# Optimization experiments

Measured on AMD Instinct MI355X. Metric: run time of the kernel, lower is better.

Reference implementation:

```python
import jax, jax.numpy as jnp
import numpy as np

DIM = 128
H = 8
EXP = 4
INNER = EXP * DIM          # 512
HD = INNER // H            # 64
B, N = 4, 1024
PE_C = 32


def setup_inputs() -> dict:
    key = jax.random.key(0)
    ks = jax.random.split(key, 9)
    s = 0.02
    return {
        "x": jax.random.normal(ks[0], (B, N, DIM), jnp.float32),
        "pe": jax.random.normal(ks[1], (N, N, PE_C), jnp.float32),
        "Wq": jax.random.normal(ks[2], (INNER, DIM), jnp.float32) * s,
        "Wk": jax.random.normal(ks[3], (INNER, DIM), jnp.float32) * s,
        "Wv": jax.random.normal(ks[4], (INNER, DIM), jnp.float32) * s,
        "bv": jax.random.normal(ks[5], (INNER,), jnp.float32) * s,
        "Wproj": jax.random.normal(ks[6], (DIM, INNER), jnp.float32) * s,
        "Wpe": jax.random.normal(ks[7], (HD, PE_C), jnp.float32) * s,
        "bpe": jax.random.normal(ks[8], (HD,), jnp.float32) * s,
    }


def reference(x, pe, Wq, Wk, Wv, bv, Wproj, Wpe, bpe):
    Bsz, Nn, C = x.shape
    scale = HD ** (-0.5)
    # [B, N, inner] -> [B, H, N, hd]
    def split_heads(t):
        return t.reshape(Bsz, Nn, H, HD).transpose(0, 2, 1, 3)
    q = split_heads(x @ Wq.T)
    k = split_heads(x @ Wk.T)
    v = split_heads(x @ Wv.T + bv)
    score = jnp.einsum('bhic,bhjc->bhij', q * scale, k)   # [B,H,N,N]
    attn = jax.nn.softmax(score, axis=-1)
    out = jnp.einsum('bhij,bhjc->bhic', attn, v)           # [B,H,N,hd]
    pe_sum = jnp.einsum('bhij,ijc->bhic', attn, pe)        # [B,H,N,32]
    out = out + pe_sum @ Wpe.T + bpe                       # pe_proj
    out = out.transpose(0, 2, 1, 3).reshape(Bsz, Nn, H * HD)
    return out @ Wproj.T                                   # [B,N,dim]
```

## Files before the change

kernel.cpp:

```cpp
#include <hip/hip_runtime.h>
#include <hip/hip_bf16.h>

#define DIM   128
#define NH    8
#define INNER 512
#define HD    64
#define BSZ   4
#define NSEQ  1024
#define PEC   32
#define BH    32

typedef __attribute__((ext_vector_type(4))) float f32x4;
typedef __attribute__((ext_vector_type(2))) float f32x2;
typedef __attribute__((ext_vector_type(8))) short s16x8;
typedef __attribute__((ext_vector_type(4))) unsigned short u16x4;
typedef __attribute__((ext_vector_type(2))) unsigned int u32x2;
typedef __attribute__((ext_vector_type(4))) unsigned int u32x4;

__device__ __forceinline__ unsigned short f2bf(float f) {
    unsigned u = __float_as_uint(f);
    u += 0x7fffu + ((u >> 16) & 1u);
    return (unsigned short)(u >> 16);
}

__device__ __forceinline__ float bf2f(short s) {
    return __uint_as_float(((unsigned)(unsigned short)s) << 16);
}

__device__ __forceinline__ s16x8 load8bf(const float* p) {
    f32x4 a = *(const f32x4*)p;
    f32x4 b = *(const f32x4*)(p + 4);
    s16x8 r;
    r[0] = (short)f2bf(a[0]); r[1] = (short)f2bf(a[1]);
    r[2] = (short)f2bf(a[2]); r[3] = (short)f2bf(a[3]);
    r[4] = (short)f2bf(b[0]); r[5] = (short)f2bf(b[1]);
    r[6] = (short)f2bf(b[2]); r[7] = (short)f2bf(b[3]);
    return r;
}

__device__ __forceinline__ f32x4 mfma16(s16x8 a, s16x8 b, f32x4 c) {
    return __builtin_amdgcn_mfma_f32_16x16x32_bf16(a, b, c, 0, 0, 0);
}

__global__ __launch_bounds__(256) void k_qkv(
    const float* __restrict__ x,
    const float* __restrict__ Wq, const float* __restrict__ Wk,
    const float* __restrict__ Wv, const float* __restrict__ bv,
    unsigned short* __restrict__ qws, unsigned short* __restrict__ kws,
    unsigned short* __restrict__ vtws)
{
    __shared__ unsigned short xs[64][136];
    int lane = threadIdx.x & 63, wave = threadIdx.x >> 6;
    int lr = lane & 15, lg = lane >> 4;
    int ct   = blockIdx.x * 4 + wave;
    int col0 = ct * 16;
    int m0   = blockIdx.y * 64;

    int tid = threadIdx.x;
    #pragma unroll
    for (int it = 0; it < 4; ++it) {
        int flat = it * 256 + tid;
        int r = flat >> 4, c8 = (flat & 15) * 8;
        *(s16x8*)&xs[r][c8] = load8bf(x + (m0 + r) * DIM + c8);
    }
    __syncthreads();

    const float* W; int cbase; int which = col0 >> 9;
    if (which == 0)      { W = Wq; cbase = col0; }
    else if (which == 1) { W = Wk; cbase = col0 - 512; }
    else                 { W = Wv; cbase = col0 - 1024; }

    const float* wrow = W + (cbase + lr) * DIM;
    s16x8 bfr[4];
    #pragma unroll
    for (int kt = 0; kt < 4; ++kt) bfr[kt] = load8bf(wrow + kt * 32 + lg * 8);

    if (which == 2) {
        int colW = cbase + lr;
        int h = colW >> 6, d = colW & 63;
        float bias = bv[colW];
        #pragma unroll
        for (int ms = 0; ms < 4; ++ms) {
            f32x4 acc = {0.f, 0.f, 0.f, 0.f};
            #pragma unroll
            for (int kt = 0; kt < 4; ++kt) {
                s16x8 a = *(const s16x8*)&xs[ms * 16 + lr][kt * 32 + lg * 8];
                acc = mfma16(a, bfr[kt], acc);
            }
            int mB = m0 + ms * 16 + lg * 4;
            int b  = mB >> 10;
            int bh = b * NH + h;
            u16x4 pk;
            #pragma unroll
            for (int v = 0; v < 4; ++v) pk[v] = f2bf(acc[v] + bias);
            int n0 = mB & 1023;
            *(u16x4*)(vtws + (bh * HD + d) * NSEQ + n0) = pk;
        }
    } else {
        int h = cbase >> 6;
        int dbase = (cbase & 63) + lg * 4;
        unsigned short* dst = (which == 0) ? qws : kws;
        float scale = (which == 0) ? 0.125f : 1.0f;
        #pragma unroll
        for (int ms = 0; ms < 4; ++ms) {
            f32x4 acc = {0.f, 0.f, 0.f, 0.f};
            #pragma unroll
            for (int kt = 0; kt < 4; ++kt) {
                s16x8 a = *(const s16x8*)&xs[ms * 16 + lr][kt * 32 + lg * 8];
                acc = mfma16(bfr[kt], a, acc);
            }
            int m = m0 + ms * 16 + lr;
            int b = m >> 10, n = m & 1023;
            int bh = b * NH + h;
            u16x4 pk;
            #pragma unroll
            for (int v = 0; v < 4; ++v) pk[v] = f2bf(acc[v] * scale);
            *(u16x4*)(dst + ((size_t)bh * NSEQ + n) * HD + dbase) = pk;
        }
    }
}

__global__ __launch_bounds__(256, 2) void k_fattn(
    const unsigned short* __restrict__ qws, const unsigned short* __restrict__ kws,
    const unsigned short* __restrict__ vtws,
    unsigned char* __restrict__ attn8, float* __restrict__ outv)
{
    __shared__ unsigned short Pl[32 * 1024];
    __shared__ float mlb[4][2][16][2];
    int lane = threadIdx.x & 63, wave = threadIdx.x >> 6;
    int lr = lane & 15, lg = lane >> 4;
    int L = blockIdx.x;
    int bh = (L & 7) * 4 + ((L >> 3) & 3);
    int i0 = (L >> 5) * 32;

    auto paddr = [&](int r, int jb) -> char* {
        unsigned mask = (unsigned)(((r & 7) << 4) | ((r & 3) << 7));
        return (char*)Pl + (unsigned)(r * 2048) + ((unsigned)jb ^ mask);
    };

    s16x8 qf[2][2];
    #pragma unroll
    for (int m = 0; m < 2; ++m) {
        const unsigned short* qrow = qws + (bh * NSEQ + i0 + m * 16 + lr) * HD;
        qf[m][0] = *(const s16x8*)(qrow + lg * 8);
        qf[m][1] = *(const s16x8*)(qrow + 32 + lg * 8);
    }

    f32x4 s[16][2];
    #pragma unroll
    for (int jc = 0; jc < 16; ++jc) {
        const unsigned short* krow =
            kws + (bh * NSEQ + wave * 256 + jc * 16 + lr) * HD + lg * 8;
        s16x8 kf0 = *(const s16x8*)(krow);
        s16x8 kf1 = *(const s16x8*)(krow + 32);
        #pragma unroll
        for (int m = 0; m < 2; ++m) {
            f32x4 acc = {0.f, 0.f, 0.f, 0.f};
            acc = mfma16(kf0, qf[m][0], acc);
            s[jc][m] = mfma16(kf1, qf[m][1], acc);
        }
    }

    float mx[2], sm[2];
    #pragma unroll
    for (int m = 0; m < 2; ++m) {
        float v = -3.0e38f;
        #pragma unroll
        for (int jc = 0; jc < 16; ++jc) {
            f32x4 t = s[jc][m];
            v = fmaxf(v, fmaxf(fmaxf(t[0], t[1]), fmaxf(t[2], t[3])));
        }
        v = fmaxf(v, __shfl_xor(v, 16));
        v = fmaxf(v, __shfl_xor(v, 32));
        mx[m] = v;
    }
    #pragma unroll
    for (int m = 0; m < 2; ++m) {
        float sum = 0.f;
        #pragma unroll
        for (int jc = 0; jc < 16; ++jc) {
            f32x4 t = s[jc][m];
            #pragma unroll
            for (int u = 0; u < 4; ++u) { t[u] = __expf(t[u] - mx[m]); sum += t[u]; }
            s[jc][m] = t;
        }
        sum += __shfl_xor(sum, 16);
        sum += __shfl_xor(sum, 32);
        sm[m] = sum;
    }
    if (lg == 0) {
        #pragma unroll
        for (int m = 0; m < 2; ++m) {
            mlb[wave][m][lr][0] = mx[m];
            mlb[wave][m][lr][1] = sm[m];
        }
    }
    __syncthreads();

    float f[2];
    #pragma unroll
    for (int m = 0; m < 2; ++m) {
        float M = -3.0e38f;
        #pragma unroll
        for (int w = 0; w < 4; ++w) M = fmaxf(M, mlb[w][m][lr][0]);
        float Ls = 0.f;
        #pragma unroll
        for (int w = 0; w < 4; ++w)
            Ls += mlb[w][m][lr][1] * __expf(mlb[w][m][lr][0] - M);
        f[m] = __expf(mx[m] - M) / Ls;
    }

    #pragma unroll
    for (int jc = 0; jc < 16; ++jc) {
        #pragma unroll
        for (int m = 0; m < 2; ++m) {
            f32x4 t = s[jc][m];
            unsigned lo = (unsigned)f2bf(t[0] * f[m]) | ((unsigned)f2bf(t[1] * f[m]) << 16);
            unsigned hi = (unsigned)f2bf(t[2] * f[m]) | ((unsigned)f2bf(t[3] * f[m]) << 16);
            u32x2 pk = {lo, hi};
            int r  = m * 16 + lr;
            int jb = (wave * 512) + (jc * 32) + (lg * 8);
            *(u32x2*)paddr(r, jb) = pk;
        }
    }
    __syncthreads();

    #pragma unroll
    for (int r8 = 0; r8 < 8; ++r8) {
        int r = wave * 8 + r8;
        s16x8 a = *(s16x8*)paddr(r, lane * 32);
        s16x8 b = *(s16x8*)paddr(r, lane * 32 + 16);
        u32x4 w;
        #pragma unroll
        for (int q = 0; q < 2; ++q) {
            s16x8 v = q ? b : a;
            #pragma unroll
            for (int dw = 0; dw < 2; ++dw) {
                unsigned pk = __builtin_amdgcn_cvt_pk_fp8_f32(
                    bf2f(v[dw * 4 + 0]) * 256.f, bf2f(v[dw * 4 + 1]) * 256.f, 0u, false);
                pk = __builtin_amdgcn_cvt_pk_fp8_f32(
                    bf2f(v[dw * 4 + 2]) * 256.f, bf2f(v[dw * 4 + 3]) * 256.f, pk, true);
                w[q * 2 + dw] = pk;
            }
        }
        *(u32x4*)(attn8 + ((size_t)(i0 + r) * BH + bh) * NSEQ + lane * 16) = w;
    }

    int d0 = wave * 16;
    const unsigned short* vrow = vtws + (bh * HD + d0 + lr) * NSEQ + lg * 8;
    f32x4 o0 = {0.f, 0.f, 0.f, 0.f};
    f32x4 o1 = {0.f, 0.f, 0.f, 0.f};
    #pragma unroll
    for (int kt = 0; kt < 32; ++kt) {
        s16x8 bf = *(const s16x8*)(vrow + kt * 32);
        s16x8 a0 = *(s16x8*)paddr(lr,      kt * 64 + lg * 16);
        s16x8 a1 = *(s16x8*)paddr(16 + lr, kt * 64 + lg * 16);
        o0 = mfma16(a0, bf, o0);
        o1 = mfma16(a1, bf, o1);
    }
    float* orow = outv + (bh * NSEQ + i0) * HD;
    #pragma unroll
    for (int v = 0; v < 4; ++v) {
        orow[(lg * 4 + v) * HD + d0 + lr]      = o0[v];
        orow[(16 + lg * 4 + v) * HD + d0 + lr] = o1[v];
    }
}

__global__ __launch_bounds__(256) void k_pe(
    const unsigned char* __restrict__ attn8, const float* __restrict__ pe,
    float* __restrict__ pes)
{
    __shared__ unsigned short pt[4][2][PEC][40];
    __shared__ float part[4][BH][PEC];
    int i = blockIdx.x;
    int lane = threadIdx.x & 63, wave = threadIdx.x >> 6;
    int lr = lane & 15, lg = lane >> 4;
    int jp = lane & 15, cg = lane >> 4;
    const float* pei = pe + (size_t)i * NSEQ * PEC;
    int jbase = wave * 256;

    s16x8 af[8][2];
    #pragma unroll
    for (int t = 0; t < 8; ++t) {
        #pragma unroll
        for (int mh = 0; mh < 2; ++mh) {
            const unsigned char* ap =
                attn8 + ((size_t)i * BH + mh * 16 + lr) * NSEQ + jbase + t * 32 + lg * 8;
            u32x2 dd = *(const u32x2*)ap;
            f32x2 p0 = __builtin_amdgcn_cvt_pk_f32_fp8(dd[0], false);
            f32x2 p1 = __builtin_amdgcn_cvt_pk_f32_fp8(dd[0], true);
            f32x2 p2 = __builtin_amdgcn_cvt_pk_f32_fp8(dd[1], false);
            f32x2 p3 = __builtin_amdgcn_cvt_pk_f32_fp8(dd[1], true);
            s16x8 fv;
            fv[0] = (short)f2bf(p0[0]); fv[1] = (short)f2bf(p0[1]);
            fv[2] = (short)f2bf(p1[0]); fv[3] = (short)f2bf(p1[1]);
            fv[4] = (short)f2bf(p2[0]); fv[5] = (short)f2bf(p2[1]);
            fv[6] = (short)f2bf(p3[0]); fv[7] = (short)f2bf(p3[1]);
            af[t][mh] = fv;
        }
    }

    f32x4 r0, r1, r2, r3;
    auto issue = [&](int t) {
        const float* s0 = pei + (size_t)(jbase + t * 32 + jp * 2) * PEC + cg * 8;
        r0 = *(const f32x4*)(s0);
        r1 = *(const f32x4*)(s0 + 4);
        r2 = *(const f32x4*)(s0 + PEC);
        r3 = *(const f32x4*)(s0 + PEC + 4);
    };
    auto commit = [&](int buf) {
        #pragma unroll
        for (int cc = 0; cc < 4; ++cc) {
            unsigned lo = f2bf(r0[cc]), hi = f2bf(r2[cc]);
            *(unsigned*)&pt[wave][buf][cg * 8 + cc][jp * 2] = lo | (hi << 16);
        }
        #pragma unroll
        for (int cc = 0; cc < 4; ++cc) {
            unsigned lo = f2bf(r1[cc]), hi = f2bf(r3[cc]);
            *(unsigned*)&pt[wave][buf][cg * 8 + 4 + cc][jp * 2] = lo | (hi << 16);
        }
    };

    f32x4 acc00 = {0.f,0.f,0.f,0.f}, acc01 = {0.f,0.f,0.f,0.f};
    f32x4 acc10 = {0.f,0.f,0.f,0.f}, acc11 = {0.f,0.f,0.f,0.f};

    issue(0); commit(0);
    issue(1);
    #pragma unroll
    for (int t = 0; t < 8; ++t) {
        int cur = t & 1;
        s16x8 bf0 = *(const s16x8*)&pt[wave][cur][lr][lg * 8];
        s16x8 bf1 = *(const s16x8*)&pt[wave][cur][16 + lr][lg * 8];
        acc00 = mfma16(af[t][0], bf0, acc00);
        acc01 = mfma16(af[t][0], bf1, acc01);
        acc10 = mfma16(af[t][1], bf0, acc10);
        acc11 = mfma16(af[t][1], bf1, acc11);
        if (t < 7) {
            commit(cur ^ 1);
            if (t < 6) issue(t + 2);
        }
    }

    #pragma unroll
    for (int v = 0; v < 4; ++v) {
        part[wave][lg * 4 + v][lr]           = acc00[v];
        part[wave][lg * 4 + v][16 + lr]      = acc01[v];
        part[wave][16 + lg * 4 + v][lr]      = acc10[v];
        part[wave][16 + lg * 4 + v][16 + lr] = acc11[v];
    }
    __syncthreads();

    int tid = threadIdx.x;
    int bh = tid >> 3, c0 = (tid & 7) * 4;
    f32x4 s = *(f32x4*)&part[0][bh][c0];
    #pragma unroll
    for (int w = 1; w < 4; ++w) {
        f32x4 q = *(f32x4*)&part[w][bh][c0];
        s[0] += q[0]; s[1] += q[1]; s[2] += q[2]; s[3] += q[3];
    }
    const float inv256 = 1.0f / 256.0f;
    s[0] *= inv256; s[1] *= inv256; s[2] *= inv256; s[3] *= inv256;
    *(f32x4*)(pes + ((size_t)bh * NSEQ + i) * PEC + c0) = s;
}

__global__ __launch_bounds__(512) void k_out(
    const float* __restrict__ outv, const float* __restrict__ pes,
    const float* __restrict__ Wpe, const float* __restrict__ bpe,
    const float* __restrict__ Wproj, float* __restrict__ out)
{
    __shared__ float wpe_s[HD * PEC];
    __shared__ float bpe_s[HD];
    __shared__ unsigned short tl[16][520];
    int tid = threadIdx.x;
    for (int idx = tid; idx < HD * PEC; idx += 512) wpe_s[idx] = Wpe[idx];
    if (tid < HD) bpe_s[tid] = bpe[tid];
    __syncthreads();

    int m0 = blockIdx.x * 16;

    {
        int r  = tid >> 5;
        int o  = tid & 31;
        int d0 = (o & 7) * 8;
        int hp = o >> 3;
        int m  = m0 + r;
        int b  = m >> 10, n = m & 1023;
        #pragma unroll
        for (int hh = 0; hh < 2; ++hh) {
            int h  = hh * 4 + hp;
            int bh = b * NH + h;
            const float* prow = pes + ((size_t)bh * NSEQ + n) * PEC;
            float pr[PEC];
            #pragma unroll
            for (int c = 0; c < PEC; c += 4) {
                f32x4 t = *(const f32x4*)(prow + c);
                pr[c] = t[0]; pr[c+1] = t[1]; pr[c+2] = t[2]; pr[c+3] = t[3];
            }
            const float* ovp = outv + ((size_t)bh * NSEQ + n) * HD + d0;
            s16x8 pk;
            #pragma unroll
            for (int dd = 0; dd < 8; ++dd) {
                float acc = bpe_s[d0 + dd] + ovp[dd];
                const float* wr = &wpe_s[(d0 + dd) * PEC];
                #pragma unroll
                for (int c = 0; c < PEC; ++c) acc += pr[c] * wr[c];
                pk[dd] = (short)f2bf(acc);
            }
            *(s16x8*)&tl[r][h * HD + d0] = pk;
        }
    }
    __syncthreads();

    int lane = tid & 63, wave = tid >> 6;
    int lr = lane & 15, lg = lane >> 4;
    int n0 = wave * 16;
    const float* brow = Wproj + (n0 + lr) * INNER;
    f32x4 acc = {0.f, 0.f, 0.f, 0.f};
    #pragma unroll
    for (int kt = 0; kt < 16; ++kt) {
        s16x8 afr = *(const s16x8*)&tl[lr][kt * 32 + lg * 8];
        s16x8 bfr = load8bf(brow + kt * 32 + lg * 8);
        acc = mfma16(afr, bfr, acc);
    }
    #pragma unroll
    for (int v = 0; v < 4; ++v)
        out[(m0 + lg * 4 + v) * DIM + n0 + lr] = acc[v];
}

extern "C" void kernel_launch(void* const* d_in, const int* in_sizes, int n_in,
                              void* d_out, int out_size, void* d_ws, size_t ws_size,
                              hipStream_t stream)
{
    const float* x     = (const float*)d_in[0];
    const float* pe    = (const float*)d_in[1];
    const float* Wq    = (const float*)d_in[2];
    const float* Wk    = (const float*)d_in[3];
    const float* Wv    = (const float*)d_in[4];
    const float* bv    = (const float*)d_in[5];
    const float* Wproj = (const float*)d_in[6];
    const float* Wpe   = (const float*)d_in[7];
    const float* bpe   = (const float*)d_in[8];
    float* out = (float*)d_out;

    char* ws = (char*)d_ws;
    unsigned short* qws  = (unsigned short*)(ws);
    unsigned short* kws  = (unsigned short*)(ws + ( 4u << 20));
    unsigned short* vtws = (unsigned short*)(ws + ( 8u << 20));
    unsigned char*  attn = (unsigned char*) (ws + (12u << 20));
    float*          outv = (float*)         (ws + (76u << 20));
    float*          pes  = (float*)         (ws + (84u << 20));

    k_qkv  <<<dim3(24, 64), 256, 0, stream>>>(x, Wq, Wk, Wv, bv, qws, kws, vtws);
    k_fattn<<<dim3(1024),   256, 0, stream>>>(qws, kws, vtws, attn, outv);
    k_pe   <<<dim3(1024),   256, 0, stream>>>(attn, pe, pes);
    k_out  <<<dim3(256),    512, 0, stream>>>(outv, pes, Wpe, bpe, Wproj, out);
}
```

Before: 117.9 us.

## Fuse pe-sum reduction with pe projection and output projection kernel

Merges k_pe and k_out into one kernel, k_peout, so each query-row block takes its pe_sum straight from shared memory. It then adds the Wpe projection and bias to outv and runs the Wproj GEMM for that row across all 4 batches. This removes one kernel launch and the global write and read of the pes buffer, and shared memory is reused across the phases. The cost is that every one of the 1024 blocks now re-reads the full Wproj matrix, four times the previous Wproj traffic. The MFMA also runs a 16-row tile of which only 4 rows are valid, so most of that matrix work is wasted.

```diff
diff --git a/kernel.cpp b/kernel.cpp
--- a/kernel.cpp
+++ b/kernel.cpp
@@ -266,14 +266,20 @@
     }
 }
 
-__global__ __launch_bounds__(256) void k_pe(
+__global__ __launch_bounds__(256) void k_peout(
     const unsigned char* __restrict__ attn8, const float* __restrict__ pe,
-    float* __restrict__ pes)
+    const float* __restrict__ outv,
+    const float* __restrict__ Wpe, const float* __restrict__ bpe,
+    const float* __restrict__ Wproj, float* __restrict__ out)
 {
-    __shared__ unsigned short pt[4][2][PEC][40];
-    __shared__ float part[4][BH][PEC];
+    __shared__ char smem[36 * 1024];
+    typedef unsigned short ptrow_t[2][PEC][40];
+    ptrow_t* pt = (ptrow_t*)smem;
+    float (*part)[BH][PEC] = (float (*)[BH][PEC])(smem + 20480);
+
     int i = blockIdx.x;
-    int lane = threadIdx.x & 63, wave = threadIdx.x >> 6;
+    int tid = threadIdx.x;
+    int lane = tid & 63, wave = tid >> 6;
     int lr = lane & 15, lg = lane >> 4;
     int jp = lane & 15, cg = lane >> 4;
     const float* pei = pe + (size_t)i * NSEQ * PEC;
@@ -350,81 +356,68 @@
     }
     __syncthreads();
 
-    int tid = threadIdx.x;
-    int bh = tid >> 3, c0 = (tid & 7) * 4;
-    f32x4 s = *(f32x4*)&part[0][bh][c0];
+    int bhr = tid >> 3, c0 = (tid & 7) * 4;
+    f32x4 s = *(f32x4*)&part[0][bhr][c0];
     #pragma unroll
     for (int w = 1; w < 4; ++w) {
-        f32x4 q = *(f32x4*)&part[w][bh][c0];
+        f32x4 q = *(f32x4*)&part[w][bhr][c0];
         s[0] += q[0]; s[1] += q[1]; s[2] += q[2]; s[3] += q[3];
     }
     const float inv256 = 1.0f / 256.0f;
     s[0] *= inv256; s[1] *= inv256; s[2] *= inv256; s[3] *= inv256;
-    *(f32x4*)(pes + ((size_t)bh * NSEQ + i) * PEC + c0) = s;
-}
-
-__global__ __launch_bounds__(512) void k_out(
-    const float* __restrict__ outv, const float* __restrict__ pes,
-    const float* __restrict__ Wpe, const float* __restrict__ bpe,
-    const float* __restrict__ Wproj, float* __restrict__ out)
-{
-    __shared__ float wpe_s[HD * PEC];
-    __shared__ float bpe_s[HD];
-    __shared__ unsigned short tl[16][520];
-    int tid = threadIdx.x;
-    for (int idx = tid; idx < HD * PEC; idx += 512) wpe_s[idx] = Wpe[idx];
+    __syncthreads();
+
+    float (*pes_s)[33] = (float (*)[33])(smem + 20480);
+    float (*wpe_s)[33] = (float (*)[33])(smem + 20480 + 4224);
+    float* bpe_s = (float*)(smem + 20480 + 4224 + 8448);
+    #pragma unroll
+    for (int v = 0; v < 4; ++v) pes_s[bhr][c0 + v] = s[v];
+    for (int idx = tid; idx < HD * PEC; idx += 256)
+        wpe_s[idx >> 5][idx & 31] = Wpe[idx];
     if (tid < HD) bpe_s[tid] = bpe[tid];
     __syncthreads();
 
-    int m0 = blockIdx.x * 16;
-
+    unsigned short (*tl)[520] = (unsigned short (*)[520])smem;
     {
-        int r  = tid >> 5;
-        int o  = tid & 31;
-        int d0 = (o & 7) * 8;
-        int hp = o >> 3;
-        int m  = m0 + r;
-        int b  = m >> 10, n = m & 1023;
-        #pragma unroll
-        for (int hh = 0; hh < 2; ++hh) {
-            int h  = hh * 4 + hp;
-            int bh = b * NH + h;
-            const float* prow = pes + ((size_t)bh * NSEQ + n) * PEC;
-            float pr[PEC];
-            #pragma unroll
-            for (int c = 0; c < PEC; c += 4) {
-                f32x4 t = *(const f32x4*)(prow + c);
-                pr[c] = t[0]; pr[c+1] = t[1]; pr[c+2] = t[2]; pr[c+3] = t[3];
-            }
-            const float* ovp = outv + ((size_t)bh * NSEQ + n) * HD + d0;
-            s16x8 pk;
-            #pragma unroll
-            for (int dd = 0; dd < 8; ++dd) {
-                float acc = bpe_s[d0 + dd] + ovp[dd];
-                const float* wr = &wpe_s[(d0 + dd) * PEC];
-                #pragma unroll
-                for (int c = 0; c < PEC; ++c) acc += pr[c] * wr[c];
-                pk[dd] = (short)f2bf(acc);
-            }
-            *(s16x8*)&tl[r][h * HD + d0] = pk;
-        }
-    }
-    __syncthreads();
-
-    int lane = tid & 63, wave = tid >> 6;
-    int lr = lane & 15, lg = lane >> 4;
-    int n0 = wave * 16;
-    const float* brow = Wproj + (n0 + lr) * INNER;
-    f32x4 acc = {0.f, 0.f, 0.f, 0.f};
-    #pragma unroll
-    for (int kt = 0; kt < 16; ++kt) {
-        s16x8 afr = *(const s16x8*)&tl[lr][kt * 32 + lg * 8];
-        s16x8 bfr = load8bf(brow + kt * 32 + lg * 8);
-        acc = mfma16(afr, bfr, acc);
-    }
-    #pragma unroll
-    for (int v = 0; v < 4; ++v)
-        out[(m0 + lg * 4 + v) * DIM + n0 + lr] = acc[v];
+        int b  = tid >> 6;
+        int h  = (tid >> 3) & 7;
+        int d0 = (tid & 7) * 8;
+        int bh = b * NH + h;
+        const float* ovp = outv + ((size_t)bh * NSEQ + i) * HD + d0;
+        f32x4 ov0 = *(const f32x4*)(ovp);
+        f32x4 ov1 = *(const f32x4*)(ovp + 4);
+        float pr[PEC];
+        #pragma unroll
+        for (int c = 0; c < PEC; ++c) pr[c] = pes_s[bh][c];
+        s16x8 pk;
+        #pragma unroll
+        for (int dd = 0; dd < 8; ++dd) {
+            float acc = bpe_s[d0 + dd] + (dd < 4 ? ov0[dd & 3] : ov1[dd & 3]);
+            #pragma unroll
+            for (int c = 0; c < PEC; ++c) acc += pr[c] * wpe_s[d0 + dd][c];
+            pk[dd] = (short)f2bf(acc);
+        }
+        *(s16x8*)&tl[b][h * HD + d0] = pk;
+    }
+    __syncthreads();
+
+    #pragma unroll
+    for (int nt = 0; nt < 2; ++nt) {
+        int n0 = wave * 32 + nt * 16;
+        const float* brow = Wproj + (n0 + lr) * INNER;
+        f32x4 acc = {0.f, 0.f, 0.f, 0.f};
+        #pragma unroll
+        for (int kt = 0; kt < 16; ++kt) {
+            s16x8 afr = *(const s16x8*)&tl[lr][kt * 32 + lg * 8];
+            s16x8 bfr = load8bf(brow + kt * 32 + lg * 8);
+            acc = mfma16(afr, bfr, acc);
+        }
+        if (lg == 0) {
+            #pragma unroll
+            for (int v = 0; v < 4; ++v)
+                out[((size_t)(v * NSEQ + i)) * DIM + n0 + lr] = acc[v];
+        }
+    }
 }
 
 extern "C" void kernel_launch(void* const* d_in, const int* in_sizes, int n_in,
@@ -447,11 +440,9 @@
     unsigned short* kws  = (unsigned short*)(ws + ( 4u << 20));
     unsigned short* vtws = (unsigned short*)(ws + ( 8u << 20));
     unsigned char*  attn = (unsigned char*) (ws + (12u << 20));
-    float*          outv = (float*)         (ws + (76u << 20));
-    float*          pes  = (float*)         (ws + (84u << 20));
+    float*          outv = (float*)         (ws + (44u << 20));
 
     k_qkv  <<<dim3(24, 64), 256, 0, stream>>>(x, Wq, Wk, Wv, bv, qws, kws, vtws);
     k_fattn<<<dim3(1024),   256, 0, stream>>>(qws, kws, vtws, attn, outv);
-    k_pe   <<<dim3(1024),   256, 0, stream>>>(attn, pe, pes);
-    k_out  <<<dim3(256),    512, 0, stream>>>(outv, pes, Wpe, bpe, Wproj, out);
-}
+    k_peout<<<dim3(1024),   256, 0, stream>>>(attn, pe, outv, Wpe, bpe, Wproj, out);
+}
```

New measurement: 113.9 us (median of 2 runs). 3.3% less time.

## Split PE aggregation across four j-quarters and reduce partials in output kernel

Applied to the files above, without the earlier changes.

The positional-encoding aggregation kernel now launches four blocks per query row. Each block covers one quarter of the key dimension, and each wave handles two tiles instead of eight. Partial sums go to four separate buffers, and the output kernel sums them while loading. This raises grid parallelism and shortens each block's serial pipeline on the pe-bandwidth-bound stage. The cost is four times the partial-sum writes and extra reads in the output kernel.

```diff
diff --git a/kernel.cpp b/kernel.cpp
--- a/kernel.cpp
+++ b/kernel.cpp
@@ -266,22 +266,24 @@
     }
 }
 
-__global__ __launch_bounds__(256) void k_pe(
+__global__ __launch_bounds__(256) void k_pe4(
     const unsigned char* __restrict__ attn8, const float* __restrict__ pe,
-    float* __restrict__ pes)
+    float* __restrict__ pesp)
 {
     __shared__ unsigned short pt[4][2][PEC][40];
     __shared__ float part[4][BH][PEC];
-    int i = blockIdx.x;
-    int lane = threadIdx.x & 63, wave = threadIdx.x >> 6;
+    int L = blockIdx.x;
+    int i = L >> 2, jq = L & 3;
+    int tid = threadIdx.x;
+    int lane = tid & 63, wave = tid >> 6;
     int lr = lane & 15, lg = lane >> 4;
     int jp = lane & 15, cg = lane >> 4;
     const float* pei = pe + (size_t)i * NSEQ * PEC;
-    int jbase = wave * 256;
-
-    s16x8 af[8][2];
-    #pragma unroll
-    for (int t = 0; t < 8; ++t) {
+    int jbase = jq * 256 + wave * 64;
+
+    s16x8 af[2][2];
+    #pragma unroll
+    for (int t = 0; t < 2; ++t) {
         #pragma unroll
         for (int mh = 0; mh < 2; ++mh) {
             const unsigned char* ap =
@@ -327,7 +329,7 @@
     issue(0); commit(0);
     issue(1);
     #pragma unroll
-    for (int t = 0; t < 8; ++t) {
+    for (int t = 0; t < 2; ++t) {
         int cur = t & 1;
         s16x8 bf0 = *(const s16x8*)&pt[wave][cur][lr][lg * 8];
         s16x8 bf1 = *(const s16x8*)&pt[wave][cur][16 + lr][lg * 8];
@@ -335,10 +337,7 @@
         acc01 = mfma16(af[t][0], bf1, acc01);
         acc10 = mfma16(af[t][1], bf0, acc10);
         acc11 = mfma16(af[t][1], bf1, acc11);
-        if (t < 7) {
-            commit(cur ^ 1);
-            if (t < 6) issue(t + 2);
-        }
+        if (t == 0) commit(1);
     }
 
     #pragma unroll
@@ -350,7 +349,6 @@
     }
     __syncthreads();
 
-    int tid = threadIdx.x;
     int bh = tid >> 3, c0 = (tid & 7) * 4;
     f32x4 s = *(f32x4*)&part[0][bh][c0];
     #pragma unroll
@@ -360,11 +358,13 @@
     }
     const float inv256 = 1.0f / 256.0f;
     s[0] *= inv256; s[1] *= inv256; s[2] *= inv256; s[3] *= inv256;
-    *(f32x4*)(pes + ((size_t)bh * NSEQ + i) * PEC + c0) = s;
+    float* dst = pesp + (size_t)jq * BH * NSEQ * PEC
+                      + ((size_t)bh * NSEQ + i) * PEC + c0;
+    *(f32x4*)dst = s;
 }
 
 __global__ __launch_bounds__(512) void k_out(
-    const float* __restrict__ outv, const float* __restrict__ pes,
+    const float* __restrict__ outv, const float* __restrict__ pesp,
     const float* __restrict__ Wpe, const float* __restrict__ bpe,
     const float* __restrict__ Wproj, float* __restrict__ out)
 {
@@ -377,6 +377,7 @@
     __syncthreads();
 
     int m0 = blockIdx.x * 16;
+    const size_t Q = (size_t)BH * NSEQ * PEC;
 
     {
         int r  = tid >> 5;
@@ -389,12 +390,18 @@
         for (int hh = 0; hh < 2; ++hh) {
             int h  = hh * 4 + hp;
             int bh = b * NH + h;
-            const float* prow = pes + ((size_t)bh * NSEQ + n) * PEC;
+            const float* prow = pesp + ((size_t)bh * NSEQ + n) * PEC;
             float pr[PEC];
             #pragma unroll
             for (int c = 0; c < PEC; c += 4) {
-                f32x4 t = *(const f32x4*)(prow + c);
-                pr[c] = t[0]; pr[c+1] = t[1]; pr[c+2] = t[2]; pr[c+3] = t[3];
+                f32x4 t0 = *(const f32x4*)(prow + c);
+                f32x4 t1 = *(const f32x4*)(prow + Q + c);
+                f32x4 t2 = *(const f32x4*)(prow + 2 * Q + c);
+                f32x4 t3 = *(const f32x4*)(prow + 3 * Q + c);
+                pr[c]   = t0[0] + t1[0] + t2[0] + t3[0];
+                pr[c+1] = t0[1] + t1[1] + t2[1] + t3[1];
+                pr[c+2] = t0[2] + t1[2] + t2[2] + t3[2];
+                pr[c+3] = t0[3] + t1[3] + t2[3] + t3[3];
             }
             const float* ovp = outv + ((size_t)bh * NSEQ + n) * HD + d0;
             s16x8 pk;
@@ -447,11 +454,11 @@
     unsigned short* kws  = (unsigned short*)(ws + ( 4u << 20));
     unsigned short* vtws = (unsigned short*)(ws + ( 8u << 20));
     unsigned char*  attn = (unsigned char*) (ws + (12u << 20));
-    float*          outv = (float*)         (ws + (76u << 20));
-    float*          pes  = (float*)         (ws + (84u << 20));
+    float*          outv = (float*)         (ws + (44u << 20));
+    float*          pesp = (float*)         (ws + (52u << 20));
 
     k_qkv  <<<dim3(24, 64), 256, 0, stream>>>(x, Wq, Wk, Wv, bv, qws, kws, vtws);
     k_fattn<<<dim3(1024),   256, 0, stream>>>(qws, kws, vtws, attn, outv);
-    k_pe   <<<dim3(1024),   256, 0, stream>>>(attn, pe, pes);
-    k_out  <<<dim3(256),    512, 0, stream>>>(outv, pes, Wpe, bpe, Wproj, out);
-}
+    k_pe4  <<<dim3(4096),   256, 0, stream>>>(attn, pe, pesp);
+    k_out  <<<dim3(256),    512, 0, stream>>>(outv, pesp, Wpe, bpe, Wproj, out);
+}
```

New measurement: 120.3 us. 2.1% more time.
